# Performance work log

Measured on AMD Instinct MI355X. Metric: run time of the kernel, lower is better.

The kernel has to match this reference:

```python
import jax, jax.numpy as jnp
import numpy as np

B, T, D, H, L = 8, 128, 400, 300, 45  # batch, max_length, 2*word_lstm_size, hidden, tag_count


def setup_inputs() -> dict:
    key = jax.random.key(0)
    ks = jax.random.split(key, 10)
    s = 0.05
    return {
        "cont_repr": jax.random.normal(ks[0], (B, T, D), jnp.float32),
        "root": jax.random.normal(ks[1], (1, 1, D), jnp.float32),
        "W1a": jax.random.normal(ks[2], (D, H), jnp.float32) * s,
        "W1b": jax.random.normal(ks[3], (D, H), jnp.float32) * s,
        "b1": jnp.zeros((H,), jnp.float32),
        "Wa": jax.random.normal(ks[4], (H, 1), jnp.float32) * s,
        "ba": jnp.zeros((1,), jnp.float32),
        "Wl": jax.random.normal(ks[5], (H, L), jnp.float32) * s,
        "bl": jnp.zeros((L,), jnp.float32),
        "sentence_lengths": jax.random.randint(ks[6], (B,), 0, T + 1),
        "desired_arcs": jax.random.randint(ks[7], (B, T), 0, T + 1),
        "desired_labels": jax.random.randint(ks[8], (B, T), 0, L),
        "use_desired_arcs": 1,
    }


def reference(cont_repr, root, W1a, W1b, b1, Wa, ba, Wl, bl,
              sentence_lengths, desired_arcs, desired_labels, use_desired_arcs):
    b, t, d = cont_repr.shape
    mask = (jnp.arange(t)[None, :] < sentence_lengths[:, None]).astype(cont_repr.dtype)  # [B,T]
    n_valid = jnp.maximum(mask.sum(), 1.0)

    # Dense(concat(tile_a, tile_b)) == tile_a @ W1a + tile_b @ W1b (exact same math,
    # avoids materializing the [B,T,T+1,2D] concat the TF graph builds).
    a_proj = jnp.einsum('btd,dh->bth', cont_repr, W1a)                     # [B,T,H]
    with_root = jnp.concatenate([jnp.broadcast_to(root, (b, 1, d)), cont_repr], axis=1)  # [B,T+1,D]
    b_proj = jnp.einsum('bsd,dh->bsh', with_root, W1b)                     # [B,T+1,H]
    h = jax.nn.relu(a_proj[:, :, None, :] + b_proj[:, None, :, :] + b1)    # [B,T,T+1,H]

    # UAS: arc scorer (units=1) over T+1 head candidates
    arc_logits = jnp.einsum('btsh,ho->btso', h, Wa)[..., 0] + ba[0]        # [B,T,T+1]
    predicted_arcs = jnp.argmax(arc_logits, axis=-1)                        # [B,T]
    arc_logp = jax.nn.log_softmax(arc_logits, axis=-1)
    arc_ce = -jnp.take_along_axis(arc_logp, desired_arcs[..., None], axis=-1)[..., 0]
    uas_loss = (arc_ce * mask).sum() / n_valid

    # LAS: gather pair repr at selected head, score labels
    sel = desired_arcs if use_desired_arcs else predicted_arcs             # [B,T]
    idx = jnp.broadcast_to(sel[:, :, None, None], (b, t, 1, h.shape[-1]))
    sel_h = jnp.take_along_axis(h, idx, axis=2)[:, :, 0, :]                # [B,T,H]
    lab_logits = jnp.einsum('bth,hl->btl', sel_h, Wl) + bl                 # [B,T,L]
    lab_logp = jax.nn.log_softmax(lab_logits, axis=-1)
    lab_ce = -jnp.take_along_axis(lab_logp, desired_labels[..., None], axis=-1)[..., 0]
    las_loss = (lab_ce * mask).sum() / n_valid

    return (uas_loss + las_loss) / 2
```

## Files before the change

kernel.cpp:

```cpp
#include <hip/hip_runtime.h>
#include <hip/hip_bf16.h>
#include <math.h>

#define BN 8
#define TT 128
#define DD 400
#define HH 300
#define LL 45
#define SS 129
#define ALG_STRIDE 132
#define PADW 308

__global__ __launch_bounds__(320, 1) void proj_kernel(
    const float* __restrict__ cont, const float* __restrict__ root,
    const float* __restrict__ W1a, const float* __restrict__ W1b,
    const float* __restrict__ b1,
    const int* __restrict__ slen,
    float* __restrict__ AP, float* __restrict__ BPX,
    float* __restrict__ accum)
{
    const int blk = blockIdx.x;
    const int tid = threadIdx.x;
    const int h   = tid;
    const bool hok = (h < HH);

    if (blk == 256) {
        if (tid == 0) accum[0] = 0.f;
        if (hok) {
            const float* wp = W1b + h;
            float acc = 0.f;
            #pragma unroll
            for (int dc = 0; dc < DD; dc += 4) {
                const float w0 = wp[(size_t)(dc + 0) * HH];
                const float w1 = wp[(size_t)(dc + 1) * HH];
                const float w2 = wp[(size_t)(dc + 2) * HH];
                const float w3 = wp[(size_t)(dc + 3) * HH];
                acc = fmaf(root[dc + 0], w0, acc);
                acc = fmaf(root[dc + 1], w1, acc);
                acc = fmaf(root[dc + 2], w2, acc);
                acc = fmaf(root[dc + 3], w3, acc);
            }
            #pragma unroll
            for (int bb = 0; bb < BN; ++bb)
                BPX[(size_t)bb * SS * HH + h] = acc;
        }
        return;
    }

    const bool isA = (blk < 128);
    const int u    = isA ? blk : blk - 128;
    const int row0 = u * 8;
    if (isA) {
        if ((row0 & 127) >= slen[row0 >> 7]) return;
    }
    if (!hok) return;

    const float* wp   = (isA ? W1a : W1b) + h;
    const float* rows = cont + (size_t)row0 * DD;

    float acc[8];
    #pragma unroll
    for (int r = 0; r < 8; ++r) acc[r] = 0.f;

    #pragma unroll
    for (int dc = 0; dc < DD; dc += 4) {
        const float w0 = wp[(size_t)(dc + 0) * HH];
        const float w1 = wp[(size_t)(dc + 1) * HH];
        const float w2 = wp[(size_t)(dc + 2) * HH];
        const float w3 = wp[(size_t)(dc + 3) * HH];
        #pragma unroll
        for (int r = 0; r < 8; ++r) {
            const float* rp = rows + r * DD + dc;
            acc[r] = fmaf(rp[0], w0, acc[r]);
            acc[r] = fmaf(rp[1], w1, acc[r]);
            acc[r] = fmaf(rp[2], w2, acc[r]);
            acc[r] = fmaf(rp[3], w3, acc[r]);
        }
    }

    if (isA) {
        const float bb = b1[h];
        float* dst = AP + (size_t)row0 * HH + h;
        #pragma unroll
        for (int r = 0; r < 8; ++r) dst[(size_t)r * HH] = acc[r] + bb;
    } else {
        const int b = row0 >> 7, t = row0 & 127;
        float* dst = BPX + ((size_t)(b * SS + t + 1)) * HH + h;
        #pragma unroll
        for (int r = 0; r < 8; ++r) dst[(size_t)r * HH] = acc[r];
    }
}

__global__ __launch_bounds__(256) void arc_kernel(
    const float* __restrict__ AP, const float* __restrict__ BPX,
    const float* __restrict__ Wa, const int* __restrict__ slen,
    float* __restrict__ ALG)
{
    __shared__ float ap_s[8][PADW];
    __shared__ float bp_s[33][PADW];
    __shared__ float wa_s[PADW];

    const int blk = blockIdx.x;
    const int b  = blk >> 6;
    const int tt = (blk >> 2) & 15;
    const int sc = blk & 3;
    const int t0 = tt * 8;
    if (t0 >= slen[b]) return;

    const int tid  = threadIdx.x;
    const int lane = tid & 63;
    const int wave = tid >> 6;
    const int tl   = lane & 7;
    const int sl   = lane >> 3;
    const int s0   = sc * 32;

    {
        const float* apg = AP + (size_t)(b * TT + t0) * HH;
        for (int i = tid; i < 8 * HH; i += 256)
            ap_s[i / HH][i % HH] = apg[i];
        const float* bpg = BPX + (size_t)(b * SS + s0) * HH;
        for (int i = tid; i < 33 * HH; i += 256)
            bp_s[i / HH][i % HH] = bpg[i];
        for (int i = tid; i < HH; i += 256)
            wa_s[i] = Wa[i];
    }
    __syncthreads();

    const int s_local = wave * 8 + sl;
    const float* aprow = ap_s[tl];
    const float* bprow = bp_s[s_local];

    float acc = 0.f;
    #pragma unroll 5
    for (int hh = 0; hh < HH; hh += 4) {
        const float4 a4 = *(const float4*)&aprow[hh];
        const float4 p4 = *(const float4*)&bprow[hh];
        const float4 w4 = *(const float4*)&wa_s[hh];
        acc = fmaf(fmaxf(a4.x + p4.x, 0.f), w4.x, acc);
        acc = fmaf(fmaxf(a4.y + p4.y, 0.f), w4.y, acc);
        acc = fmaf(fmaxf(a4.z + p4.z, 0.f), w4.z, acc);
        acc = fmaf(fmaxf(a4.w + p4.w, 0.f), w4.w, acc);
    }
    ALG[(size_t)(b * TT + t0 + tl) * ALG_STRIDE + s0 + s_local] = acc;

    if (sc == 3 && wave == 0 && sl == 0) {
        const float* bpr = bp_s[32];
        float a2 = 0.f;
        #pragma unroll 5
        for (int hh = 0; hh < HH; hh += 4) {
            const float4 a4 = *(const float4*)&aprow[hh];
            const float4 p4 = *(const float4*)&bpr[hh];
            const float4 w4 = *(const float4*)&wa_s[hh];
            a2 = fmaf(fmaxf(a4.x + p4.x, 0.f), w4.x, a2);
            a2 = fmaf(fmaxf(a4.y + p4.y, 0.f), w4.y, a2);
            a2 = fmaf(fmaxf(a4.z + p4.z, 0.f), w4.z, a2);
            a2 = fmaf(fmaxf(a4.w + p4.w, 0.f), w4.w, a2);
        }
        ALG[(size_t)(b * TT + t0 + tl) * ALG_STRIDE + 128] = a2;
    }
}

__global__ __launch_bounds__(256) void smx_kernel(
    const float* __restrict__ AP, const float* __restrict__ BPX,
    const float* __restrict__ Wl, const float* __restrict__ bl,
    const float* __restrict__ ALG,
    const int* __restrict__ slen, const int* __restrict__ des_arcs,
    const int* __restrict__ des_labels, const int* __restrict__ use_des,
    float* __restrict__ accum)
{
    const int blk = blockIdx.x;
    const int b = blk >> 7, t = blk & 127;
    if (t >= slen[b]) return;
    const int tid  = threadIdx.x;
    const int lane = tid & 63;
    const int wave = tid >> 6;

    __shared__ float selh[HH];
    __shared__ float partial[4][64];
    __shared__ float arc_ce_s;
    __shared__ int   sel_s;

    if (wave == 0) {
        const float* lg = ALG + (size_t)blk * ALG_STRIDE;
        const float v0 = lg[lane];
        const float v1 = lg[64 + lane];
        const float v2 = (lane == 0) ? lg[128] : -INFINITY;

        float m = fmaxf(fmaxf(v0, v1), v2);
        #pragma unroll
        for (int off = 32; off; off >>= 1) m = fmaxf(m, __shfl_xor(m, off, 64));
        float e = __expf(v0 - m) + __expf(v1 - m) + ((lane == 0) ? __expf(v2 - m) : 0.f);
        #pragma unroll
        for (int off = 32; off; off >>= 1) e += __shfl_xor(e, off, 64);
        const float arc_lse = m + __logf(e);

        float bv = v0; int bi = lane;
        if (v1 > bv) { bv = v1; bi = 64 + lane; }
        if (lane == 0 && v2 > bv) { bv = v2; bi = 128; }
        #pragma unroll
        for (int off = 32; off; off >>= 1) {
            const float ov = __shfl_xor(bv, off, 64);
            const int   oi = __shfl_xor(bi, off, 64);
            if (ov > bv || (ov == bv && oi < bi)) { bv = ov; bi = oi; }
        }
        if (lane == 0) {
            const int da = des_arcs[b * TT + t];
            arc_ce_s = arc_lse - lg[da];
            sel_s = use_des[0] ? da : bi;
        }
    }
    __syncthreads();

    {
        const int sel = sel_s;
        const float* ap = AP + (size_t)blk * HH;
        const float* bp = BPX + (size_t)(b * SS + sel) * HH;
        for (int hh = tid; hh < HH; hh += 256)
            selh[hh] = fmaxf(ap[hh] + bp[hh], 0.f);
    }
    __syncthreads();

    {
        float p = 0.f;
        if (lane < LL) {
            const int h0 = wave * 75;
            #pragma unroll 5
            for (int j = 0; j < 75; ++j)
                p = fmaf(selh[h0 + j], Wl[(h0 + j) * LL + lane], p);
        }
        partial[wave][lane] = p;
    }
    __syncthreads();

    if (wave == 0) {
        float a = -INFINITY;
        if (lane < LL)
            a = bl[lane] + partial[0][lane] + partial[1][lane]
                         + partial[2][lane] + partial[3][lane];
        float lm = a;
        #pragma unroll
        for (int off = 32; off; off >>= 1) lm = fmaxf(lm, __shfl_xor(lm, off, 64));
        float le = (lane < LL) ? __expf(a - lm) : 0.f;
        #pragma unroll
        for (int off = 32; off; off >>= 1) le += __shfl_xor(le, off, 64);
        const float lab_lse = lm + __logf(le);

        const int dl = des_labels[b * TT + t];
        const float ldl = __shfl(a, dl, 64);
        if (lane == 0)
            atomicAdd(accum, arc_ce_s + (lab_lse - ldl));
    }
}

__global__ void finalize_kernel(const float* __restrict__ accum,
                                const int* __restrict__ slen,
                                float* __restrict__ out)
{
    if (threadIdx.x == 0) {
        int n = 0;
        for (int b = 0; b < BN; ++b) {
            int l = slen[b];
            if (l < 0) l = 0;
            if (l > TT) l = TT;
            n += l;
        }
        float nv = (float)n;
        if (nv < 1.f) nv = 1.f;
        out[0] = accum[0] / (2.f * nv);
    }
}

extern "C" void kernel_launch(void* const* d_in, const int* in_sizes, int n_in,
                              void* d_out, int out_size, void* d_ws, size_t ws_size,
                              hipStream_t stream) {
    const float* cont = (const float*)d_in[0];
    const float* root = (const float*)d_in[1];
    const float* W1a  = (const float*)d_in[2];
    const float* W1b  = (const float*)d_in[3];
    const float* b1   = (const float*)d_in[4];
    const float* Wa   = (const float*)d_in[5];
    const float* Wl   = (const float*)d_in[7];
    const float* bl   = (const float*)d_in[8];
    const int* slen   = (const int*)d_in[9];
    const int* darc   = (const int*)d_in[10];
    const int* dlab   = (const int*)d_in[11];
    const int* used   = (const int*)d_in[12];
    float* out = (float*)d_out;

    float* AP    = (float*)d_ws;
    float* BPX   = AP  + 1024 * HH;
    float* ALG   = BPX + BN * SS * HH;
    float* accum = ALG + 1024 * ALG_STRIDE;

    proj_kernel<<<257, 320, 0, stream>>>(cont, root, W1a, W1b, b1, slen, AP, BPX, accum);
    arc_kernel<<<512, 256, 0, stream>>>(AP, BPX, Wa, slen, ALG);
    smx_kernel<<<1024, 256, 0, stream>>>(AP, BPX, Wl, bl, ALG, slen, darc, dlab, used, accum);
    finalize_kernel<<<1, 64, 0, stream>>>(accum, slen, out);
}
```

Measured before the change: 50.99 us.

## Split projection K-dimension across two thread groups with LDS-staged rows

The projection kernel now uses 640 threads per block: two groups of 320 each handle half of the 400-wide reduction dimension, and their partial sums are combined through shared memory. The 8 input rows plus the root vector are staged into LDS and read as float4, instead of each thread reading them from global memory. The separate root-projection block is folded into block 128 as a ninth row, which removes one block and the serial 400-step loop it ran. The cost is an extra LDS reduction, two extra barriers, and nine accumulators held per thread, which raises register pressure.

Result: slower. 53.99 us (+5.9%).

```diff
diff --git a/kernel.cpp b/kernel.cpp
--- a/kernel.cpp
+++ b/kernel.cpp
@@ -11,7 +11,7 @@
 #define ALG_STRIDE 132
 #define PADW 308
 
-__global__ __launch_bounds__(320, 1) void proj_kernel(
+__global__ __launch_bounds__(640) void proj_kernel(
     const float* __restrict__ cont, const float* __restrict__ root,
     const float* __restrict__ W1a, const float* __restrict__ W1b,
     const float* __restrict__ b1,
@@ -19,75 +19,81 @@
     float* __restrict__ AP, float* __restrict__ BPX,
     float* __restrict__ accum)
 {
+    __shared__ float rows_s[9 * DD];
     const int blk = blockIdx.x;
     const int tid = threadIdx.x;
-    const int h   = tid;
+
+    const bool isA   = (blk < 128);
+    const bool isRB  = (blk == 128);
+    const int  u     = isA ? blk : blk - 128;
+    const int  row0  = u * 8;
+
+    if (isRB && tid == 0) accum[0] = 0.f;
+    if (isA && ((row0 & 127) >= slen[row0 >> 7])) return;
+
+    {
+        const float* src = cont + (size_t)row0 * DD;
+        for (int i = tid; i < 8 * DD; i += 640) rows_s[i] = src[i];
+        for (int i = tid; i < DD; i += 640)     rows_s[8 * DD + i] = root[i];
+    }
+    __syncthreads();
+
+    const int grp = tid / 320;
+    const int h   = tid % 320;
     const bool hok = (h < HH);
 
-    if (blk == 256) {
-        if (tid == 0) accum[0] = 0.f;
-        if (hok) {
-            const float* wp = W1b + h;
-            float acc = 0.f;
+    float acc[9];
+    #pragma unroll
+    for (int r = 0; r < 9; ++r) acc[r] = 0.f;
+
+    if (hok) {
+        const float* wp = (isA ? W1a : W1b) + (size_t)(grp * 200) * HH + h;
+        const float* rs = rows_s;
+        const int dbase = grp * 200;
+        #pragma unroll
+        for (int dc = 0; dc < 200; dc += 4) {
+            const float w0 = wp[(size_t)(dc + 0) * HH];
+            const float w1 = wp[(size_t)(dc + 1) * HH];
+            const float w2 = wp[(size_t)(dc + 2) * HH];
+            const float w3 = wp[(size_t)(dc + 3) * HH];
             #pragma unroll
-            for (int dc = 0; dc < DD; dc += 4) {
-                const float w0 = wp[(size_t)(dc + 0) * HH];
-                const float w1 = wp[(size_t)(dc + 1) * HH];
-                const float w2 = wp[(size_t)(dc + 2) * HH];
-                const float w3 = wp[(size_t)(dc + 3) * HH];
-                acc = fmaf(root[dc + 0], w0, acc);
-                acc = fmaf(root[dc + 1], w1, acc);
-                acc = fmaf(root[dc + 2], w2, acc);
-                acc = fmaf(root[dc + 3], w3, acc);
+            for (int r = 0; r < 9; ++r) {
+                const float4 ra = *(const float4*)&rs[r * DD + dbase + dc];
+                acc[r] = fmaf(ra.x, w0, acc[r]);
+                acc[r] = fmaf(ra.y, w1, acc[r]);
+                acc[r] = fmaf(ra.z, w2, acc[r]);
+                acc[r] = fmaf(ra.w, w3, acc[r]);
             }
+        }
+    }
+
+    __syncthreads();
+    float* red = rows_s;
+    if (grp == 1 && hok) {
+        #pragma unroll
+        for (int r = 0; r < 9; ++r) red[h * 9 + r] = acc[r];
+    }
+    __syncthreads();
+    if (grp == 0 && hok) {
+        float tot[9];
+        #pragma unroll
+        for (int r = 0; r < 9; ++r) tot[r] = acc[r] + red[h * 9 + r];
+        if (isA) {
+            const float bb = b1[h];
+            float* dst = AP + (size_t)row0 * HH + h;
             #pragma unroll
-            for (int bb = 0; bb < BN; ++bb)
-                BPX[(size_t)bb * SS * HH + h] = acc;
-        }
-        return;
-    }
-
-    const bool isA = (blk < 128);
-    const int u    = isA ? blk : blk - 128;
-    const int row0 = u * 8;
-    if (isA) {
-        if ((row0 & 127) >= slen[row0 >> 7]) return;
-    }
-    if (!hok) return;
-
-    const float* wp   = (isA ? W1a : W1b) + h;
-    const float* rows = cont + (size_t)row0 * DD;
-
-    float acc[8];
-    #pragma unroll
-    for (int r = 0; r < 8; ++r) acc[r] = 0.f;
-
-    #pragma unroll
-    for (int dc = 0; dc < DD; dc += 4) {
-        const float w0 = wp[(size_t)(dc + 0) * HH];
-        const float w1 = wp[(size_t)(dc + 1) * HH];
-        const float w2 = wp[(size_t)(dc + 2) * HH];
-        const float w3 = wp[(size_t)(dc + 3) * HH];
-        #pragma unroll
-        for (int r = 0; r < 8; ++r) {
-            const float* rp = rows + r * DD + dc;
-            acc[r] = fmaf(rp[0], w0, acc[r]);
-            acc[r] = fmaf(rp[1], w1, acc[r]);
-            acc[r] = fmaf(rp[2], w2, acc[r]);
-            acc[r] = fmaf(rp[3], w3, acc[r]);
-        }
-    }
-
-    if (isA) {
-        const float bb = b1[h];
-        float* dst = AP + (size_t)row0 * HH + h;
-        #pragma unroll
-        for (int r = 0; r < 8; ++r) dst[(size_t)r * HH] = acc[r] + bb;
-    } else {
-        const int b = row0 >> 7, t = row0 & 127;
-        float* dst = BPX + ((size_t)(b * SS + t + 1)) * HH + h;
-        #pragma unroll
-        for (int r = 0; r < 8; ++r) dst[(size_t)r * HH] = acc[r];
+            for (int r = 0; r < 8; ++r) dst[(size_t)r * HH] = tot[r] + bb;
+        } else {
+            const int b = row0 >> 7, t = row0 & 127;
+            float* dst = BPX + ((size_t)(b * SS + t + 1)) * HH + h;
+            #pragma unroll
+            for (int r = 0; r < 8; ++r) dst[(size_t)r * HH] = tot[r];
+            if (isRB) {
+                #pragma unroll
+                for (int bb2 = 0; bb2 < BN; ++bb2)
+                    BPX[(size_t)bb2 * SS * HH + h] = tot[8];
+            }
+        }
     }
 }
 
@@ -292,7 +298,7 @@
     float* ALG   = BPX + BN * SS * HH;
     float* accum = ALG + 1024 * ALG_STRIDE;
 
-    proj_kernel<<<257, 320, 0, stream>>>(cont, root, W1a, W1b, b1, slen, AP, BPX, accum);
+    proj_kernel<<<256, 640, 0, stream>>>(cont, root, W1a, W1b, b1, slen, AP, BPX, accum);
     arc_kernel<<<512, 256, 0, stream>>>(AP, BPX, Wa, slen, ALG);
     smx_kernel<<<1024, 256, 0, stream>>>(AP, BPX, Wl, bl, ALG, slen, darc, dlab, used, accum);
     finalize_kernel<<<1, 64, 0, stream>>>(accum, slen, out);
```
